# Performance work log

Hardware: AMD Instinct MI355X
Metric: run time of the kernel (lower is better)

Reference implementation:

```python
import jax, jax.numpy as jnp
import numpy as np

I = 6156  # input feature size
O = 3     # output classes
B = 2048  # batch


def setup_inputs() -> dict:
    key = jax.random.key(0)
    ks = jax.random.split(key, 6)
    x = jax.random.normal(ks[0], (B, I), dtype=jnp.float32)
    # nn.Linear(input_size, output_size)
    lin_w = jax.random.normal(ks[1], (O, I), dtype=jnp.float32) * (1.0 / np.sqrt(I))
    lin_b = jax.random.normal(ks[2], (O,), dtype=jnp.float32) * 0.01
    # interaction_weights: xavier_uniform_ on (I, I)
    limit = float(np.sqrt(6.0 / (I + I)))
    w_int = jax.random.uniform(ks[3], (I, I), dtype=jnp.float32, minval=-limit, maxval=limit)
    # final_layer: nn.Linear(I + O, O)
    fin_w = jax.random.normal(ks[4], (O, I + O), dtype=jnp.float32) * (1.0 / np.sqrt(I + O))
    fin_b = jax.random.normal(ks[5], (O,), dtype=jnp.float32) * 0.01
    return {"x": x, "lin_w": lin_w, "lin_b": lin_b, "w_int": w_int,
            "fin_w": fin_w, "fin_b": fin_b}


def reference(x, lin_w, lin_b, w_int, fin_w, fin_b):
    # linear_logits = x @ lin_w.T + lin_b  -> [B, O]
    linear_logits = x @ lin_w.T + lin_b
    # einsum('bi,bj,ij->bij').sum(dim=2) == x * (x @ w_int.T)
    # GEMM [B,I]x[I,I] + elementwise multiply; no O(B*I*I) intermediate.
    interactions = x * (x @ w_int.T)  # [B, I]
    combined = jnp.concatenate([linear_logits, interactions], axis=1)  # [B, O+I]
    logits = combined @ fin_w.T + fin_b  # [B, O]
    return logits
```

## Files before the change

### kernel.cpp

```cpp
#include <hip/hip_runtime.h>
#include <hip/hip_bf16.h>

constexpr int Bsz = 2048;
constexpr int Iin = 6156;
constexpr int IF  = 6159;
constexpr int Kp  = 6208;
constexpr int NpW = 6400;
constexpr int NTI = Kp / 64;

typedef __attribute__((ext_vector_type(8))) short short8;
typedef __attribute__((ext_vector_type(4))) float f32x4;
typedef __attribute__((ext_vector_type(4))) int   i32x4;

#define AS1 __attribute__((address_space(1)))
#define AS3 __attribute__((address_space(3)))

__device__ __forceinline__ short f2bf(float f) {
    union { float f; unsigned u; } v; v.f = f;
    unsigned r = v.u + 0x7FFFu + ((v.u >> 16) & 1u);
    return (short)(r >> 16);
}

__device__ __forceinline__ short8 pack8(float4 a, float4 b) {
    short8 r;
    r[0] = f2bf(a.x); r[1] = f2bf(a.y); r[2] = f2bf(a.z); r[3] = f2bf(a.w);
    r[4] = f2bf(b.x); r[5] = f2bf(b.y); r[6] = f2bf(b.z); r[7] = f2bf(b.w);
    return r;
}

__device__ __forceinline__ void stage_chunk(const void* src, const void* ldsbase) {
    __builtin_amdgcn_global_load_lds((const AS1 void*)src, (AS3 void*)ldsbase, 16, 0, 0);
}

__global__ void linear_init_kernel(const float* __restrict__ x,
                                   const float* __restrict__ lin_w,
                                   const float* __restrict__ lin_b,
                                   const float* __restrict__ fin_w,
                                   const float* __restrict__ fin_b,
                                   float* __restrict__ out) {
    int wid  = threadIdx.x >> 6;
    int lane = threadIdx.x & 63;
    int b = blockIdx.x * 4 + wid;
    if (b >= Bsz) return;
    const float4* xr = (const float4*)(x + (size_t)b * Iin);
    const float4* w0 = (const float4*)(lin_w);
    const float4* w1 = (const float4*)(lin_w + Iin);
    const float4* w2 = (const float4*)(lin_w + 2 * Iin);
    float s0 = 0.f, s1 = 0.f, s2 = 0.f;
    for (int i = lane; i < Iin / 4; i += 64) {
        float4 xv = xr[i];
        float4 a0 = w0[i], a1 = w1[i], a2 = w2[i];
        s0 += xv.x * a0.x + xv.y * a0.y + xv.z * a0.z + xv.w * a0.w;
        s1 += xv.x * a1.x + xv.y * a1.y + xv.z * a1.z + xv.w * a1.w;
        s2 += xv.x * a2.x + xv.y * a2.y + xv.z * a2.z + xv.w * a2.w;
    }
    #pragma unroll
    for (int off = 1; off < 64; off <<= 1) {
        s0 += __shfl_xor(s0, off, 64);
        s1 += __shfl_xor(s1, off, 64);
        s2 += __shfl_xor(s2, off, 64);
    }
    if (lane == 0) {
        float l0 = s0 + lin_b[0], l1 = s1 + lin_b[1], l2 = s2 + lin_b[2];
        #pragma unroll
        for (int o = 0; o < 3; ++o) {
            out[b * 3 + o] = fin_b[o]
                + fin_w[(size_t)o * IF + 0] * l0
                + fin_w[(size_t)o * IF + 1] * l1
                + fin_w[(size_t)o * IF + 2] * l2;
        }
    }
}

__global__ __launch_bounds__(256) void quant_kernel(
    const float* __restrict__ src, signed char* __restrict__ dst,
    float* __restrict__ scales, int src_rows) {
    __shared__ float rowbuf[Kp];
    __shared__ float red[4];
    int row = blockIdx.x;
    int t   = threadIdx.x;
    float amax = 0.f;
    if (row < src_rows) {
        const float4* s = (const float4*)(src + (size_t)row * Iin);
        for (int i = t; i < Iin / 4; i += 256) {
            float4 v = s[i];
            ((float4*)rowbuf)[i] = v;
            amax = fmaxf(amax, fmaxf(fmaxf(fabsf(v.x), fabsf(v.y)),
                                     fmaxf(fabsf(v.z), fabsf(v.w))));
        }
        for (int i = Iin + t; i < Kp; i += 256) rowbuf[i] = 0.f;
    } else {
        for (int i = t; i < Kp; i += 256) rowbuf[i] = 0.f;
    }
    #pragma unroll
    for (int off = 1; off < 64; off <<= 1)
        amax = fmaxf(amax, __shfl_xor(amax, off, 64));
    if ((t & 63) == 0) red[t >> 6] = amax;
    __syncthreads();
    float am = fmaxf(fmaxf(red[0], red[1]), fmaxf(red[2], red[3]));
    float rs = (am > 0.f) ? 127.f / am : 0.f;
    if (t == 0) scales[row] = (am > 0.f) ? am / 127.f : 0.f;

    int xorv = (row >> 1) & 3;
    for (int p = t; p < Kp / 16; p += 256) {
        int blk = p >> 2, sub = p & 3;
        int sc  = (blk << 6) + ((sub ^ xorv) << 4);
        i32x4 pk;
        #pragma unroll
        for (int j = 0; j < 4; ++j) {
            unsigned u = 0;
            #pragma unroll
            for (int e = 0; e < 4; ++e) {
                float v = rowbuf[sc + j * 4 + e] * rs;
                int q = (int)rintf(v);
                q = q > 127 ? 127 : (q < -127 ? -127 : q);
                u |= ((unsigned)(q & 255)) << (8 * e);
            }
            pk[j] = (int)u;
        }
        *(i32x4*)(dst + (size_t)row * Kp + (size_t)p * 16) = pk;
    }
}

__global__ __launch_bounds__(512, 4) void gemm_i8t(
    const signed char* __restrict__ xq, const signed char* __restrict__ wq,
    const float* __restrict__ sx, const float* __restrict__ sw,
    const float* __restrict__ xf, const float* __restrict__ finw,
    float* __restrict__ out) {

    __shared__ signed char lsA[2][16384];
    __shared__ signed char lsB[2][8192];
    __shared__ float part[256][3];

    const int tid  = threadIdx.x;
    const int lane = tid & 63;
    const int wid  = tid >> 6;
    const int wr   = wid >> 1;
    const int wc   = wid & 1;
    const int l15  = lane & 15;
    const int koff = (((lane >> 4) ^ ((lane >> 1) & 3)) << 4);

    const int tm = (int)blockIdx.x & 7;
    const int tn = (int)blockIdx.x >> 3;
    const int bm0 = tm << 8;
    const int in0 = tn << 7;

    i32x4 acc[4][4];
    #pragma unroll
    for (int m = 0; m < 4; ++m)
        #pragma unroll
        for (int n = 0; n < 4; ++n)
            acc[m][n] = (i32x4){0, 0, 0, 0};

    auto stageA = [&](int tk) {
        #pragma unroll
        for (int j = 0; j < 2; ++j) {
            int idx = j * 512 + tid;
            int row = idx >> 2, sub = idx & 3;
            const signed char* src = xq + (size_t)(bm0 + row) * Kp + tk * 64 + sub * 16;
            stage_chunk(src, &lsA[tk & 1][(size_t)idx * 16]);
        }
    };
    auto stageB = [&](int tk) {
        int row = tid >> 2, sub = tid & 3;
        const signed char* src = wq + (size_t)(in0 + row) * Kp + tk * 64 + sub * 16;
        stage_chunk(src, &lsB[tk & 1][(size_t)tid * 16]);
    };
    auto ldA = [&](int slot, int m) -> i32x4 {
        int row = wr * 64 + m * 16 + l15;
        return *(const i32x4*)&lsA[slot][row * 64 + koff];
    };
    auto ldB = [&](int slot, int n) -> i32x4 {
        int row = wc * 64 + n * 16 + l15;
        return *(const i32x4*)&lsB[slot][row * 64 + koff];
    };

    stageA(0); stageB(0);

    for (int t = 0; t < NTI; ++t) {
        asm volatile("s_waitcnt vmcnt(0)" ::: "memory");
        __builtin_amdgcn_s_barrier();
        __builtin_amdgcn_sched_barrier(0);
        if (t + 1 < NTI) { stageA(t + 1); stageB(t + 1); }
        __builtin_amdgcn_sched_barrier(0);

        const int sl = t & 1;
        i32x4 af[4], bf[4];
        #pragma unroll
        for (int m = 0; m < 4; ++m) af[m] = ldA(sl, m);
        #pragma unroll
        for (int n = 0; n < 4; ++n) bf[n] = ldB(sl, n);
        #pragma unroll
        for (int m = 0; m < 4; ++m)
            #pragma unroll
            for (int n = 0; n < 4; ++n)
                acc[m][n] = __builtin_amdgcn_mfma_i32_16x16x64_i8(
                    af[m], bf[n], acc[m][n], 0, 0, 0);
    }

    __syncthreads();
    for (int t = tid; t < 768; t += 512) ((float*)part)[t] = 0.f;
    __syncthreads();

    int q4 = lane >> 4;
    #pragma unroll
    for (int m = 0; m < 4; ++m) {
        #pragma unroll
        for (int r = 0; r < 4; ++r) {
            int lr = wr * 64 + m * 16 + q4 * 4 + r;
            int bg = bm0 + lr;
            float sxv = sx[bg];
            float s0 = 0.f, s1 = 0.f, s2 = 0.f;
            #pragma unroll
            for (int n = 0; n < 4; ++n) {
                int gi = in0 + wc * 64 + n * 16 + l15;
                if (gi < Iin) {
                    float z = (float)acc[m][n][r] * sxv * sw[gi];
                    float inter = z * xf[(size_t)bg * Iin + gi];
                    s0 += inter * finw[(size_t)0 * IF + 3 + gi];
                    s1 += inter * finw[(size_t)1 * IF + 3 + gi];
                    s2 += inter * finw[(size_t)2 * IF + 3 + gi];
                }
            }
            #pragma unroll
            for (int off = 1; off < 16; off <<= 1) {
                s0 += __shfl_xor(s0, off, 64);
                s1 += __shfl_xor(s1, off, 64);
                s2 += __shfl_xor(s2, off, 64);
            }
            if (l15 == 0) {
                atomicAdd(&part[lr][0], s0);
                atomicAdd(&part[lr][1], s1);
                atomicAdd(&part[lr][2], s2);
            }
        }
    }
    __syncthreads();
    for (int t = tid; t < 768; t += 512) {
        int lr = t / 3, o = t - lr * 3;
        atomicAdd(&out[(size_t)(bm0 + lr) * 3 + o], part[lr][o]);
    }
}

__global__ __launch_bounds__(256) void gemm_fallback(
    const float* __restrict__ xf, const float* __restrict__ wf,
    const float* __restrict__ finw, float* __restrict__ out) {

    __shared__ short lsA[128 * 64];
    __shared__ short lsB[128 * 64];
    __shared__ float part[128][3];

    int tid  = threadIdx.x;
    int lane = tid & 63;
    int wid  = tid >> 6;
    int wm   = wid & 1;
    int wn   = wid >> 1;

    int ntiles = (Bsz / 128) * (6272 / 128);
    int tile = (blockIdx.x & 7) * (ntiles >> 3) + (blockIdx.x >> 3);
    int tm = tile & 15;
    int tn = tile >> 4;
    int bm0 = tm << 7;
    int in0 = tn << 7;

    f32x4 acc[4][4];
    #pragma unroll
    for (int m = 0; m < 4; ++m)
        #pragma unroll
        for (int n = 0; n < 4; ++n)
            acc[m][n] = (f32x4){0.f, 0.f, 0.f, 0.f};

    for (int k0 = 0; k0 < Kp; k0 += 64) {
        #pragma unroll
        for (int it = 0; it < 4; ++it) {
            int idx = it * 256 + tid;
            int r   = idx >> 3;
            int seg = idx & 7;
            int kc  = k0 + seg * 8;
            int sd  = (seg ^ (r & 7)) << 3;
            {
                const float* s = xf + (size_t)(bm0 + r) * Iin + kc;
                short8 st;
                if (kc + 8 <= Iin) {
                    float4 f0 = *(const float4*)s;
                    float4 f1 = *(const float4*)(s + 4);
                    st = pack8(f0, f1);
                } else {
                    #pragma unroll
                    for (int e = 0; e < 8; ++e) {
                        float v = (kc + e < Iin) ? s[e] : 0.f;
                        st[e] = f2bf(v);
                    }
                }
                *(short8*)&lsA[r * 64 + sd] = st;
            }
            {
                int grow = in0 + r;
                short8 st;
                if (grow < Iin && kc + 8 <= Iin) {
                    const float* s = wf + (size_t)grow * Iin + kc;
                    float4 f0 = *(const float4*)s;
                    float4 f1 = *(const float4*)(s + 4);
                    st = pack8(f0, f1);
                } else if (grow < Iin) {
                    const float* s = wf + (size_t)grow * Iin + kc;
                    #pragma unroll
                    for (int e = 0; e < 8; ++e) {
                        float v = (kc + e < Iin) ? s[e] : 0.f;
                        st[e] = f2bf(v);
                    }
                } else {
                    #pragma unroll
                    for (int e = 0; e < 8; ++e) st[e] = 0;
                }
                *(short8*)&lsB[r * 64 + sd] = st;
            }
        }
        __syncthreads();

        #pragma unroll
        for (int kk = 0; kk < 2; ++kk) {
            int q = (kk << 2) + (lane >> 4);
            short8 af[4], bfr[4];
            #pragma unroll
            for (int m = 0; m < 4; ++m) {
                int R = wm * 64 + m * 16 + (lane & 15);
                af[m] = *(const short8*)&lsA[R * 64 + ((q ^ (R & 7)) << 3)];
            }
            #pragma unroll
            for (int n = 0; n < 4; ++n) {
                int R = wn * 64 + n * 16 + (lane & 15);
                bfr[n] = *(const short8*)&lsB[R * 64 + ((q ^ (R & 7)) << 3)];
            }
            #pragma unroll
            for (int m = 0; m < 4; ++m)
                #pragma unroll
                for (int n = 0; n < 4; ++n)
                    acc[m][n] = __builtin_amdgcn_mfma_f32_16x16x32_bf16(
                        af[m], bfr[n], acc[m][n], 0, 0, 0);
        }
        __syncthreads();
    }

    for (int t = tid; t < 384; t += 256) ((float*)part)[t] = 0.f;
    __syncthreads();

    #pragma unroll
    for (int m = 0; m < 4; ++m) {
        int rowbase = bm0 + wm * 64 + m * 16 + ((lane >> 4) << 2);
        #pragma unroll
        for (int r = 0; r < 4; ++r) {
            int b = rowbase + r;
            float s0 = 0.f, s1 = 0.f, s2 = 0.f;
            #pragma unroll
            for (int n = 0; n < 4; ++n) {
                int gi = in0 + wn * 64 + n * 16 + (lane & 15);
                if (gi < Iin) {
                    float inter = acc[m][n][r] * xf[(size_t)b * Iin + gi];
                    s0 += inter * finw[(size_t)0 * IF + 3 + gi];
                    s1 += inter * finw[(size_t)1 * IF + 3 + gi];
                    s2 += inter * finw[(size_t)2 * IF + 3 + gi];
                }
            }
            #pragma unroll
            for (int off = 1; off < 16; off <<= 1) {
                s0 += __shfl_xor(s0, off, 64);
                s1 += __shfl_xor(s1, off, 64);
                s2 += __shfl_xor(s2, off, 64);
            }
            if ((lane & 15) == 0) {
                int lr = b - bm0;
                atomicAdd(&part[lr][0], s0);
                atomicAdd(&part[lr][1], s1);
                atomicAdd(&part[lr][2], s2);
            }
        }
    }
    __syncthreads();
    for (int t = tid; t < 384; t += 256) {
        int lr = t / 3, o = t - lr * 3;
        atomicAdd(&out[(size_t)(bm0 + lr) * 3 + o], part[lr][o]);
    }
}

extern "C" void kernel_launch(void* const* d_in, const int* in_sizes, int n_in,
                              void* d_out, int out_size, void* d_ws, size_t ws_size,
                              hipStream_t stream) {
    const float* x     = (const float*)d_in[0];
    const float* lin_w = (const float*)d_in[1];
    const float* lin_b = (const float*)d_in[2];
    const float* w_int = (const float*)d_in[3];
    const float* fin_w = (const float*)d_in[4];
    const float* fin_b = (const float*)d_in[5];
    float* out = (float*)d_out;

    linear_init_kernel<<<Bsz / 4, 256, 0, stream>>>(x, lin_w, lin_b, fin_w, fin_b, out);

    const size_t xq_bytes = (size_t)Bsz * Kp;
    const size_t wq_bytes = (size_t)NpW * Kp;
    const size_t sx_off   = xq_bytes + wq_bytes;
    const size_t need = sx_off + (Bsz + NpW) * sizeof(float);

    if (ws_size >= need) {
        signed char* xq = (signed char*)d_ws;
        signed char* wq = xq + xq_bytes;
        float* sxp = (float*)((char*)d_ws + sx_off);
        float* swp = sxp + Bsz;
        quant_kernel<<<Bsz, 256, 0, stream>>>(x, xq, sxp, Bsz);
        quant_kernel<<<NpW, 256, 0, stream>>>(w_int, wq, swp, Iin);
        gemm_i8t<<<8 * 50, 512, 0, stream>>>(xq, wq, sxp, swp, x, fin_w, out);
    } else {
        const int ntiles = (Bsz / 128) * (6272 / 128);
        gemm_fallback<<<ntiles, 256, 0, stream>>>(x, w_int, fin_w, out);
    }
}
```

Before: 181.5 us.

## Pre-pack int8 operands in MFMA fragment order and load directly to registers

```diff
diff --git a/kernel.cpp b/kernel.cpp
--- a/kernel.cpp
+++ b/kernel.cpp
@@ -6,14 +6,11 @@
 constexpr int IF  = 6159;
 constexpr int Kp  = 6208;
 constexpr int NpW = 6400;
-constexpr int NTI = Kp / 64;
+constexpr int NSEC = Kp / 64;
 
 typedef __attribute__((ext_vector_type(8))) short short8;
 typedef __attribute__((ext_vector_type(4))) float f32x4;
 typedef __attribute__((ext_vector_type(4))) int   i32x4;
-
-#define AS1 __attribute__((address_space(1)))
-#define AS3 __attribute__((address_space(3)))
 
 __device__ __forceinline__ short f2bf(float f) {
     union { float f; unsigned u; } v; v.f = f;
@@ -26,10 +23,6 @@
     r[0] = f2bf(a.x); r[1] = f2bf(a.y); r[2] = f2bf(a.z); r[3] = f2bf(a.w);
     r[4] = f2bf(b.x); r[5] = f2bf(b.y); r[6] = f2bf(b.z); r[7] = f2bf(b.w);
     return r;
-}
-
-__device__ __forceinline__ void stage_chunk(const void* src, const void* ldsbase) {
-    __builtin_amdgcn_global_load_lds((const AS1 void*)src, (AS3 void*)ldsbase, 16, 0, 0);
 }
 
 __global__ void linear_init_kernel(const float* __restrict__ x,
@@ -72,11 +65,12 @@
     }
 }
 
-__global__ __launch_bounds__(256) void quant_kernel(
+__global__ __launch_bounds__(256) void quant_pack_kernel(
     const float* __restrict__ src, signed char* __restrict__ dst,
-    float* __restrict__ scales, int src_rows) {
+    float* __restrict__ scales, int src_rows, int rsh) {
     __shared__ float rowbuf[Kp];
     __shared__ float red[4];
+    const int RPT = 1 << rsh;
     int row = blockIdx.x;
     int t   = threadIdx.x;
     float amax = 0.f;
@@ -101,35 +95,34 @@
     float rs = (am > 0.f) ? 127.f / am : 0.f;
     if (t == 0) scales[row] = (am > 0.f) ? am / 127.f : 0.f;
 
-    int xorv = (row >> 1) & 3;
+    const int rtile = row >> rsh;
+    const int rloc  = row & (RPT - 1);
     for (int p = t; p < Kp / 16; p += 256) {
-        int blk = p >> 2, sub = p & 3;
-        int sc  = (blk << 6) + ((sub ^ xorv) << 4);
+        int ts = p >> 2, ks = p & 3;
         i32x4 pk;
         #pragma unroll
         for (int j = 0; j < 4; ++j) {
             unsigned u = 0;
             #pragma unroll
             for (int e = 0; e < 4; ++e) {
-                float v = rowbuf[sc + j * 4 + e] * rs;
+                float v = rowbuf[p * 16 + j * 4 + e] * rs;
                 int q = (int)rintf(v);
                 q = q > 127 ? 127 : (q < -127 ? -127 : q);
                 u |= ((unsigned)(q & 255)) << (8 * e);
             }
             pk[j] = (int)u;
         }
-        *(i32x4*)(dst + (size_t)row * Kp + (size_t)p * 16) = pk;
-    }
-}
-
-__global__ __launch_bounds__(512, 4) void gemm_i8t(
-    const signed char* __restrict__ xq, const signed char* __restrict__ wq,
+        size_t off = ((size_t)(rtile * 97 + ts) * RPT + rloc) * 64 + ks * 16;
+        *(i32x4*)(dst + off) = pk;
+    }
+}
+
+__global__ __launch_bounds__(256) void gemm_dg(
+    const signed char* __restrict__ xqp, const signed char* __restrict__ wqp,
     const float* __restrict__ sx, const float* __restrict__ sw,
     const float* __restrict__ xf, const float* __restrict__ finw,
     float* __restrict__ out) {
 
-    __shared__ signed char lsA[2][16384];
-    __shared__ signed char lsB[2][8192];
     __shared__ float part[256][3];
 
     const int tid  = threadIdx.x;
@@ -138,76 +131,77 @@
     const int wr   = wid >> 1;
     const int wc   = wid & 1;
     const int l15  = lane & 15;
-    const int koff = (((lane >> 4) ^ ((lane >> 1) & 3)) << 4);
 
     const int tm = (int)blockIdx.x & 7;
     const int tn = (int)blockIdx.x >> 3;
     const int bm0 = tm << 8;
     const int in0 = tn << 7;
 
-    i32x4 acc[4][4];
-    #pragma unroll
-    for (int m = 0; m < 4; ++m)
+    const int laneoff = (lane & 15) * 64 + (lane >> 4) * 16;
+    const signed char* Ab = xqp + (size_t)tm * 97 * 16384 + wr * 8192 + laneoff;
+    const signed char* Bb = wqp + (size_t)tn * 97 * 8192  + wc * 4096 + laneoff;
+
+    i32x4 acc[8][4];
+    #pragma unroll
+    for (int m = 0; m < 8; ++m)
         #pragma unroll
         for (int n = 0; n < 4; ++n)
             acc[m][n] = (i32x4){0, 0, 0, 0};
 
-    auto stageA = [&](int tk) {
-        #pragma unroll
-        for (int j = 0; j < 2; ++j) {
-            int idx = j * 512 + tid;
-            int row = idx >> 2, sub = idx & 3;
-            const signed char* src = xq + (size_t)(bm0 + row) * Kp + tk * 64 + sub * 16;
-            stage_chunk(src, &lsA[tk & 1][(size_t)idx * 16]);
-        }
-    };
-    auto stageB = [&](int tk) {
-        int row = tid >> 2, sub = tid & 3;
-        const signed char* src = wq + (size_t)(in0 + row) * Kp + tk * 64 + sub * 16;
-        stage_chunk(src, &lsB[tk & 1][(size_t)tid * 16]);
-    };
-    auto ldA = [&](int slot, int m) -> i32x4 {
-        int row = wr * 64 + m * 16 + l15;
-        return *(const i32x4*)&lsA[slot][row * 64 + koff];
-    };
-    auto ldB = [&](int slot, int n) -> i32x4 {
-        int row = wc * 64 + n * 16 + l15;
-        return *(const i32x4*)&lsB[slot][row * 64 + koff];
-    };
-
-    stageA(0); stageB(0);
-
-    for (int t = 0; t < NTI; ++t) {
-        asm volatile("s_waitcnt vmcnt(0)" ::: "memory");
-        __builtin_amdgcn_s_barrier();
-        __builtin_amdgcn_sched_barrier(0);
-        if (t + 1 < NTI) { stageA(t + 1); stageB(t + 1); }
-        __builtin_amdgcn_sched_barrier(0);
-
-        const int sl = t & 1;
-        i32x4 af[4], bf[4];
-        #pragma unroll
-        for (int m = 0; m < 4; ++m) af[m] = ldA(sl, m);
-        #pragma unroll
-        for (int n = 0; n < 4; ++n) bf[n] = ldB(sl, n);
-        #pragma unroll
-        for (int m = 0; m < 4; ++m)
-            #pragma unroll
-            for (int n = 0; n < 4; ++n)
-                acc[m][n] = __builtin_amdgcn_mfma_i32_16x16x64_i8(
-                    af[m], bf[n], acc[m][n], 0, 0, 0);
-    }
-
+    i32x4 aA[8], aB[8], bA[4], bB[4];
+
+#define LDF(T, AF, BF)                                                    \
+    {                                                                     \
+        const signed char* _pa = Ab + (size_t)(T) * 16384;                \
+        _Pragma("unroll")                                                 \
+        for (int m = 0; m < 8; ++m)                                       \
+            AF[m] = *(const i32x4*)(_pa + m * 1024);                      \
+        const signed char* _pb = Bb + (size_t)(T) * 8192;                 \
+        _Pragma("unroll")                                                 \
+        for (int n = 0; n < 4; ++n)                                       \
+            BF[n] = *(const i32x4*)(_pb + n * 1024);                      \
+    }
+
+    LDF(0, aA, bA);
+    LDF(1, aB, bB);
+
+#define SECD(T, CA, CB, W, ISSUE)                                         \
+    {                                                                     \
+        asm volatile("s_waitcnt " W ::: "memory");                        \
+        __builtin_amdgcn_sched_barrier(0);                                \
+        __builtin_amdgcn_s_setprio(1);                                    \
+        _Pragma("unroll")                                                 \
+        for (int m = 0; m < 8; ++m)                                       \
+            _Pragma("unroll")                                             \
+            for (int n = 0; n < 4; ++n)                                   \
+                acc[m][n] = __builtin_amdgcn_mfma_i32_16x16x64_i8(        \
+                    CA[m], CB[n], acc[m][n], 0, 0, 0);                    \
+        __builtin_amdgcn_s_setprio(0);                                    \
+        __builtin_amdgcn_sched_barrier(0);                                \
+        if (ISSUE) LDF((T) + 2, CA, CB)                                   \
+        __builtin_amdgcn_sched_barrier(0);                                \
+    }
+
+    for (int i = 0; i < 47; ++i) {
+        int t = 2 * i;
+        SECD(t,     aA, bA, "vmcnt(12)", true);
+        SECD(t + 1, aB, bB, "vmcnt(12)", true);
+    }
+    SECD(94, aA, bA, "vmcnt(12)", true);
+    SECD(95, aB, bB, "vmcnt(12)", false);
+    SECD(96, aA, bA, "vmcnt(0)",  false);
+#undef SECD
+#undef LDF
+
+    for (int t = tid; t < 768; t += 256) ((float*)part)[t] = 0.f;
     __syncthreads();
-    for (int t = tid; t < 768; t += 512) ((float*)part)[t] = 0.f;
-    __syncthreads();
 
     int q4 = lane >> 4;
     #pragma unroll
-    for (int m = 0; m < 4; ++m) {
+    for (int m = 0; m < 8; ++m) {
         #pragma unroll
         for (int r = 0; r < 4; ++r) {
-            int lr = wr * 64 + m * 16 + q4 * 4 + r;
+            int lr = wr * 128 + m * 16 + q4 * 4 + r;
             int bg = bm0 + lr;
             float sxv = sx[bg];
             float s0 = 0.f, s1 = 0.f, s2 = 0.f;
@@ -236,7 +230,7 @@
         }
     }
     __syncthreads();
-    for (int t = tid; t < 768; t += 512) {
+    for (int t = tid; t < 768; t += 256) {
         int lr = t / 3, o = t - lr * 3;
         atomicAdd(&out[(size_t)(bm0 + lr) * 3 + o], part[lr][o]);
     }
@@ -396,19 +390,19 @@
 
     linear_init_kernel<<<Bsz / 4, 256, 0, stream>>>(x, lin_w, lin_b, fin_w, fin_b, out);
 
-    const size_t xq_bytes = (size_t)Bsz * Kp;
-    const size_t wq_bytes = (size_t)NpW * Kp;
+    const size_t xq_bytes = (size_t)8 * 97 * 16384;
+    const size_t wq_bytes = (size_t)50 * 97 * 8192;
     const size_t sx_off   = xq_bytes + wq_bytes;
     const size_t need = sx_off + (Bsz + NpW) * sizeof(float);
 
     if (ws_size >= need) {
-        signed char* xq = (signed char*)d_ws;
-        signed char* wq = xq + xq_bytes;
+        signed char* xqp = (signed char*)d_ws;
+        signed char* wqp = xqp + xq_bytes;
         float* sxp = (float*)((char*)d_ws + sx_off);
         float* swp = sxp + Bsz;
-        quant_kernel<<<Bsz, 256, 0, stream>>>(x, xq, sxp, Bsz);
-        quant_kernel<<<NpW, 256, 0, stream>>>(w_int, wq, swp, Iin);
-        gemm_i8t<<<8 * 50, 512, 0, stream>>>(xq, wq, sxp, swp, x, fin_w, out);
+        quant_pack_kernel<<<Bsz, 256, 0, stream>>>(x, xqp, sxp, Bsz, 8);
+        quant_pack_kernel<<<NpW, 256, 0, stream>>>(w_int, wqp, swp, Iin, 7);
+        gemm_dg<<<8 * 50, 256, 0, stream>>>(xqp, wqp, sxp, swp, x, fin_w, out);
     } else {
         const int ntiles = (Bsz / 128) * (6272 / 128);
         gemm_fallback<<<ntiles, 256, 0, stream>>>(x, w_int, fin_w, out);
```

New measurement: 265.7 us. +46.3%, slower.
